# Kernel tuning notes

Hardware: AMD Instinct MI355X
Metric: run time of the kernel (lower is better)

Reference implementation:

```python
import jax, jax.numpy as jnp
import numpy as np

N = 50000   # nodes
E = 600000  # edges (avg degree 12)
D = 128     # embedding_dim == hidden_features
L = 4       # depth


def setup_inputs() -> dict:
    key = jax.random.key(0)
    k0, k1, k2, k3 = jax.random.split(key, 4)
    scale = 1.0 / np.sqrt(D)
    node_embedding = jax.random.normal(k0, (N, D), jnp.float32)
    edge_index = jax.random.randint(k1, (2, E), 0, N, dtype=jnp.int32)
    Ws_rel = jax.random.normal(k2, (L, D, D), jnp.float32) * scale
    bs_rel = jnp.zeros((L, D), jnp.float32)
    Ws_root = jax.random.normal(k3, (L, D, D), jnp.float32) * scale
    return {
        'node_embedding': node_embedding,
        'edge_index': edge_index,
        'Ws_rel': Ws_rel,
        'bs_rel': bs_rel,
        'Ws_root': Ws_root,
    }


def reference(node_embedding, edge_index, Ws_rel, bs_rel, Ws_root):
    # PyG GraphConv (aggr='mean'), flow source_to_target:
    #   out_i = lin_rel(mean_{j in N(i)} x_j) + lin_root(x_i)
    # followed by ELU (dropout probs are 0 -> identity).
    n = node_embedding.shape[0]
    src, dst = edge_index[0], edge_index[1]
    ones = jnp.ones((edge_index.shape[1],), node_embedding.dtype)
    deg = jax.ops.segment_sum(ones, dst, num_segments=n)
    inv_deg = (1.0 / jnp.maximum(deg, 1.0))[:, None]  # [n, 1]
    X = node_embedding
    for l in range(Ws_rel.shape[0]):
        agg = jax.ops.segment_sum(X[src], dst, num_segments=n) * inv_deg  # [n, D]
        out = agg @ Ws_rel[l] + bs_rel[l] + X @ Ws_root[l]
        X = jax.nn.elu(out)
    return X
```

## Files before the change

### kernel.cpp

```cpp
#include <hip/hip_runtime.h>

#define D 128
#define LDR 264
#define SLOTS 64
#define EPB 2048

typedef short bf16x8 __attribute__((ext_vector_type(8)));
typedef float f32x4 __attribute__((ext_vector_type(4)));

__device__ __forceinline__ unsigned short f2bf(float f) {
  unsigned int u = __float_as_uint(f);
  unsigned int r = (u + 0x7fff + ((u >> 16) & 1)) >> 16;
  return (unsigned short)r;
}
__device__ __forceinline__ unsigned int pack2bf(float lo, float hi) {
  return (unsigned int)f2bf(lo) | ((unsigned int)f2bf(hi) << 16);
}

__global__ __launch_bounds__(256) void k_build(
    const int* __restrict__ src, const int* __restrict__ dst, int E, int N,
    int* __restrict__ cursor, unsigned short* __restrict__ csr64,
    const float* __restrict__ X0, unsigned short* __restrict__ Xb, int total4,
    const float* __restrict__ Wrel, const float* __restrict__ Wroot,
    unsigned short* __restrict__ Wp, int wtot,
    int fb, int cb) {
  int b = blockIdx.x;
  if (b < fb) {
    int p = b & 7;
    int chunk = b >> 3;
    int lo = (int)((long long)p * N / 8);
    int hi = (int)((long long)(p + 1) * N / 8);
    int base = chunk * EPB + threadIdx.x;
#pragma unroll
    for (int it = 0; it < EPB / 256; ++it, base += 256) {
      if (base < E) {
        int d = dst[base];
        if (d >= lo && d < hi) {
          int ps = atomicAdd(&cursor[d], 1);
          if (ps < SLOTS) csr64[d * SLOTS + ps] = (unsigned short)src[base];
        }
      }
    }
    return;
  }
  b -= fb;
  if (b < cb) {
    int i = b * 256 + threadIdx.x;
    if (i < total4) {
      float4 v = ((const float4*)X0)[i];
      ushort4 o;
      o.x = f2bf(v.x); o.y = f2bf(v.y); o.z = f2bf(v.z); o.w = f2bf(v.w);
      ((ushort4*)Xb)[i] = o;
    }
    return;
  }
  b -= cb;
  {
    int gid = b * 256 + threadIdx.x;
    if (gid >= wtot) return;
    int lane = gid & 63;
    int t = gid >> 6;
    int ctg = t & 7; t >>= 3;
    int ks = t & 7; t >>= 3;
    int l = t;
    const float* Wr = Wrel + (size_t)l * D * D;
    const float* Wo = Wroot + (size_t)l * D * D;
    int colc = ctg * 16 + (lane & 15);
    int krow0 = ks * 32 + (lane >> 4) * 8;
    unsigned short tmp[8];
#pragma unroll
    for (int j = 0; j < 8; ++j) {
      int kr = krow0 + j;
      float w = (kr < D) ? Wr[(size_t)kr * D + colc] : Wo[(size_t)(kr - D) * D + colc];
      tmp[j] = f2bf(w);
    }
    unsigned short* dstp = Wp + ((size_t)gid) * 8;
#pragma unroll
    for (int j = 0; j < 8; ++j) dstp[j] = tmp[j];
  }
}


#define ACC8(v) \
    acc[0] += __uint_as_float((v).x << 16); acc[1] += __uint_as_float((v).x & 0xffff0000u); \
    acc[2] += __uint_as_float((v).y << 16); acc[3] += __uint_as_float((v).y & 0xffff0000u); \
    acc[4] += __uint_as_float((v).z << 16); acc[5] += __uint_as_float((v).z & 0xffff0000u); \
    acc[6] += __uint_as_float((v).w << 16); acc[7] += __uint_as_float((v).w & 0xffff0000u);

__global__ __launch_bounds__(256) void k_aggregate(const unsigned short* __restrict__ X,
    const int* __restrict__ cursor, const unsigned short* __restrict__ csr64,
    unsigned short* __restrict__ agg, int N) {
  int wave = (int)((blockIdx.x * blockDim.x + threadIdx.x) >> 6);
  int lane = threadIdx.x & 63;
  if (wave >= N) return;
  int grp = lane >> 4;
  int l16 = lane & 15;
  int deg = cursor[wave];
  int n = min(deg, SLOTS);
  int eid = (int)csr64[wave * SLOTS + lane];

  float acc[8];
#pragma unroll
  for (int k = 0; k < 8; ++k) acc[k] = 0.f;

  int j4 = 0;
  for (; j4 + 12 <= n; j4 += 12) {
    int s0 = __shfl(eid, j4 + grp);
    int s1 = __shfl(eid, j4 + 4 + grp);
    int s2 = __shfl(eid, j4 + 8 + grp);
    uint4 v0 = *(const uint4*)(X + (size_t)s0 * D + l16 * 8);
    uint4 v1 = *(const uint4*)(X + (size_t)s1 * D + l16 * 8);
    uint4 v2 = *(const uint4*)(X + (size_t)s2 * D + l16 * 8);
    ACC8(v0) ACC8(v1) ACC8(v2)
  }
  if (j4 + 8 <= n) {
    int s0 = __shfl(eid, j4 + grp);
    int s1 = __shfl(eid, j4 + 4 + grp);
    uint4 v0 = *(const uint4*)(X + (size_t)s0 * D + l16 * 8);
    uint4 v1 = *(const uint4*)(X + (size_t)s1 * D + l16 * 8);
    ACC8(v0) ACC8(v1)
    j4 += 8;
  }
  for (; j4 < n; j4 += 4) {
    int jj = j4 + grp;
    int s = __shfl(eid, jj);
    if (jj < n) {
      uint4 v = *(const uint4*)(X + (size_t)s * D + l16 * 8);
      ACC8(v)
    }
  }

#pragma unroll
  for (int k = 0; k < 8; ++k) {
    acc[k] += __shfl_xor(acc[k], 16);
    acc[k] += __shfl_xor(acc[k], 32);
  }

  if (grp == 0) {
    float inv = 1.0f / fmaxf((float)deg, 1.0f);
    uint4 o;
    o.x = pack2bf(acc[0] * inv, acc[1] * inv);
    o.y = pack2bf(acc[2] * inv, acc[3] * inv);
    o.z = pack2bf(acc[4] * inv, acc[5] * inv);
    o.w = pack2bf(acc[6] * inv, acc[7] * inv);
    *(uint4*)(agg + (size_t)wave * D + l16 * 8) = o;
  }
}

__global__ __launch_bounds__(256, 4) void k_layer(const unsigned short* __restrict__ agg,
    const unsigned short* __restrict__ Xin, const unsigned short* __restrict__ Wp_l,
    const float* __restrict__ bias, unsigned short* __restrict__ Xnext,
    float* __restrict__ out_f32, int last, int N) {
  __shared__ __align__(16) unsigned short sRow[64 * LDR];
  int tid = threadIdx.x;
  int r0 = blockIdx.x * 64;

  for (int i = tid; i < 64 * 32; i += 256) {
    int r = i >> 5, ch = i & 31;
    int row = r0 + r;
    uint4 v = make_uint4(0, 0, 0, 0);
    if (row < N) {
      const unsigned short* srcp = (ch < 16)
          ? (agg + (size_t)row * D + ch * 8)
          : (Xin + (size_t)row * D + (ch - 16) * 8);
      v = *(const uint4*)srcp;
    }
    *(uint4*)(&sRow[r * LDR + ch * 8]) = v;
  }
  __syncthreads();

  int wave = tid >> 6, lane = tid & 63;
  int m = lane & 15, q = lane >> 4;
  int ct0 = wave * 2;

  f32x4 acc[4][2];
#pragma unroll
  for (int g = 0; g < 4; ++g)
#pragma unroll
    for (int c = 0; c < 2; ++c) acc[g][c] = (f32x4){0.f, 0.f, 0.f, 0.f};

  const unsigned short* arow = &sRow[m * LDR + q * 8];
#pragma unroll
  for (int ks = 0; ks < 8; ++ks) {
    bf16x8 b0 = *(const bf16x8*)(Wp_l + ((size_t)((ks * 8 + ct0 + 0) * 64 + lane)) * 8);
    bf16x8 b1 = *(const bf16x8*)(Wp_l + ((size_t)((ks * 8 + ct0 + 1) * 64 + lane)) * 8);
    bf16x8 a0 = *(const bf16x8*)(arow + ks * 32);
    bf16x8 a1 = *(const bf16x8*)(arow + 16 * LDR + ks * 32);
    bf16x8 a2 = *(const bf16x8*)(arow + 32 * LDR + ks * 32);
    bf16x8 a3 = *(const bf16x8*)(arow + 48 * LDR + ks * 32);
    acc[0][0] = __builtin_amdgcn_mfma_f32_16x16x32_bf16(a0, b0, acc[0][0], 0, 0, 0);
    acc[0][1] = __builtin_amdgcn_mfma_f32_16x16x32_bf16(a0, b1, acc[0][1], 0, 0, 0);
    acc[1][0] = __builtin_amdgcn_mfma_f32_16x16x32_bf16(a1, b0, acc[1][0], 0, 0, 0);
    acc[1][1] = __builtin_amdgcn_mfma_f32_16x16x32_bf16(a1, b1, acc[1][1], 0, 0, 0);
    acc[2][0] = __builtin_amdgcn_mfma_f32_16x16x32_bf16(a2, b0, acc[2][0], 0, 0, 0);
    acc[2][1] = __builtin_amdgcn_mfma_f32_16x16x32_bf16(a2, b1, acc[2][1], 0, 0, 0);
    acc[3][0] = __builtin_amdgcn_mfma_f32_16x16x32_bf16(a3, b0, acc[3][0], 0, 0, 0);
    acc[3][1] = __builtin_amdgcn_mfma_f32_16x16x32_bf16(a3, b1, acc[3][1], 0, 0, 0);
  }

#pragma unroll
  for (int g = 0; g < 4; ++g) {
#pragma unroll
    for (int c = 0; c < 2; ++c) {
      int col = (ct0 + c) * 16 + m;
      float bv = bias[col];
      int rbase = r0 + g * 16 + q * 4;
#pragma unroll
      for (int j = 0; j < 4; ++j) {
        int row = rbase + j;
        float v = acc[g][c][j] + bv;
        float e = __expf(fminf(v, 0.f)) - 1.f;
        v = v > 0.f ? v : e;
        if (last) {
          if (row < N) out_f32[(size_t)row * D + col] = v;
        } else {
          unsigned int h = (unsigned int)f2bf(v);
          unsigned int nb = (unsigned int)__shfl_xor((int)h, 1);
          if (!(m & 1) && row < N)
            *(unsigned int*)(Xnext + (size_t)row * D + col) = h | (nb << 16);
        }
      }
    }
  }
}


extern "C" void kernel_launch(void* const* d_in, const int* in_sizes, int n_in,
                              void* d_out, int out_size, void* d_ws, size_t ws_size,
                              hipStream_t stream) {
  const float* X0    = (const float*)d_in[0];
  const int*   eidx  = (const int*)d_in[1];
  const float* Wrel  = (const float*)d_in[2];
  const float* brel  = (const float*)d_in[3];
  const float* Wroot = (const float*)d_in[4];
  float* out = (float*)d_out;

  const int N = in_sizes[0] / D;
  const int E = in_sizes[1] / 2;
  const int L = in_sizes[3] / D;
  const int* src = eidx;
  const int* dst = eidx + E;

  char* ws = (char*)d_ws;
  size_t off = 0;
  auto carve = [&](size_t bytes) -> void* {
    void* p = ws + off;
    off = (off + bytes + 255) & ~(size_t)255;
    return p;
  };
  unsigned short* Xb0  = (unsigned short*)carve((size_t)N * D * sizeof(unsigned short));
  unsigned short* Xb1  = (unsigned short*)carve((size_t)N * D * sizeof(unsigned short));
  unsigned short* aggb = (unsigned short*)carve((size_t)N * D * sizeof(unsigned short));
  unsigned short* Wp   = (unsigned short*)carve((size_t)L * 4096 * 8 * sizeof(unsigned short));
  int*            cursor = (int*)carve((size_t)N * sizeof(int));
  unsigned short* csr64  = (unsigned short*)carve((size_t)N * SLOTS * sizeof(unsigned short));
  (void)ws_size; (void)n_in; (void)out_size;

  hipMemsetAsync(cursor, 0, (size_t)N * sizeof(int), stream);

  const int chunks = (E + EPB - 1) / EPB;
  const int fb = chunks * 8;
  const int total4 = N * D / 4;
  const int cb = (total4 + 255) / 256;
  const int wtot = L * 4096;
  const int wb = (wtot + 255) / 256;
  k_build<<<fb + cb + wb, 256, 0, stream>>>(src, dst, E, N, cursor, csr64,
      X0, Xb0, total4, Wrel, Wroot, Wp, wtot, fb, cb);

  const int ab = (N + 3) / 4;
  const int lb = (N + 63) / 64;

  const unsigned short* Xcur = Xb0;
  for (int l = 0; l < L; ++l) {
    int last = (l == L - 1) ? 1 : 0;
    unsigned short* Xnext = (Xcur == Xb0) ? Xb1 : Xb0;
    k_aggregate<<<ab, 256, 0, stream>>>(Xcur, cursor, csr64, aggb, N);
    k_layer<<<lb, 256, 0, stream>>>(aggb, Xcur, Wp + (size_t)l * 4096 * 8,
        brel + (size_t)l * D, Xnext, out, last, N);
    Xcur = Xnext;
  }
}
```

Measured before the change: 259.4 us.

## Assign one node per 16-lane group in aggregation instead of one per wave

```diff
diff --git a/kernel.cpp b/kernel.cpp
--- a/kernel.cpp
+++ b/kernel.cpp
@@ -90,60 +90,48 @@
 __global__ __launch_bounds__(256) void k_aggregate(const unsigned short* __restrict__ X,
     const int* __restrict__ cursor, const unsigned short* __restrict__ csr64,
     unsigned short* __restrict__ agg, int N) {
-  int wave = (int)((blockIdx.x * blockDim.x + threadIdx.x) >> 6);
+  int wid = (int)((blockIdx.x * blockDim.x + threadIdx.x) >> 6);
   int lane = threadIdx.x & 63;
-  if (wave >= N) return;
-  int grp = lane >> 4;
-  int l16 = lane & 15;
-  int deg = cursor[wave];
+  int g = lane >> 4, l16 = lane & 15;
+  int node = wid * 4 + g;
+  bool valid = node < N;
+  int nv = valid ? node : (N - 1);
+  int deg = cursor[nv];
   int n = min(deg, SLOTS);
-  int eid = (int)csr64[wave * SLOTS + lane];
+  int nmax = n;
+  nmax = max(nmax, __shfl_xor(nmax, 16));
+  nmax = max(nmax, __shfl_xor(nmax, 32));
 
   float acc[8];
 #pragma unroll
   for (int k = 0; k < 8; ++k) acc[k] = 0.f;
 
-  int j4 = 0;
-  for (; j4 + 12 <= n; j4 += 12) {
-    int s0 = __shfl(eid, j4 + grp);
-    int s1 = __shfl(eid, j4 + 4 + grp);
-    int s2 = __shfl(eid, j4 + 8 + grp);
-    uint4 v0 = *(const uint4*)(X + (size_t)s0 * D + l16 * 8);
-    uint4 v1 = *(const uint4*)(X + (size_t)s1 * D + l16 * 8);
-    uint4 v2 = *(const uint4*)(X + (size_t)s2 * D + l16 * 8);
-    ACC8(v0) ACC8(v1) ACC8(v2)
-  }
-  if (j4 + 8 <= n) {
-    int s0 = __shfl(eid, j4 + grp);
-    int s1 = __shfl(eid, j4 + 4 + grp);
-    uint4 v0 = *(const uint4*)(X + (size_t)s0 * D + l16 * 8);
-    uint4 v1 = *(const uint4*)(X + (size_t)s1 * D + l16 * 8);
-    ACC8(v0) ACC8(v1)
-    j4 += 8;
-  }
-  for (; j4 < n; j4 += 4) {
-    int jj = j4 + grp;
-    int s = __shfl(eid, jj);
-    if (jj < n) {
-      uint4 v = *(const uint4*)(X + (size_t)s * D + l16 * 8);
-      ACC8(v)
-    }
-  }
-
-#pragma unroll
-  for (int k = 0; k < 8; ++k) {
-    acc[k] += __shfl_xor(acc[k], 16);
-    acc[k] += __shfl_xor(acc[k], 32);
-  }
-
-  if (grp == 0) {
+  const unsigned short* bucket = csr64 + (size_t)nv * SLOTS;
+  for (int j0 = 0; j0 < nmax; j0 += 16) {
+    int ew = (int)bucket[j0 + l16];
+#pragma unroll
+    for (int jj = 0; jj < 16; jj += 2) {
+      int s0 = __shfl(ew, g * 16 + jj);
+      int s1 = __shfl(ew, g * 16 + jj + 1);
+      if (j0 + jj < n) {
+        uint4 v0 = *(const uint4*)(X + (size_t)s0 * D + l16 * 8);
+        ACC8(v0)
+      }
+      if (j0 + jj + 1 < n) {
+        uint4 v1 = *(const uint4*)(X + (size_t)s1 * D + l16 * 8);
+        ACC8(v1)
+      }
+    }
+  }
+
+  if (valid) {
     float inv = 1.0f / fmaxf((float)deg, 1.0f);
     uint4 o;
     o.x = pack2bf(acc[0] * inv, acc[1] * inv);
     o.y = pack2bf(acc[2] * inv, acc[3] * inv);
     o.z = pack2bf(acc[4] * inv, acc[5] * inv);
     o.w = pack2bf(acc[6] * inv, acc[7] * inv);
-    *(uint4*)(agg + (size_t)wave * D + l16 * 8) = o;
+    *(uint4*)(agg + (size_t)node * D + l16 * 8) = o;
   }
 }
 
@@ -267,7 +255,7 @@
   k_build<<<fb + cb + wb, 256, 0, stream>>>(src, dst, E, N, cursor, csr64,
       X0, Xb0, total4, Wrel, Wroot, Wp, wtot, fb, cb);
 
-  const int ab = (N + 3) / 4;
+  const int ab = (N + 15) / 16;
   const int lb = (N + 63) / 64;
 
   const unsigned short* Xcur = Xb0;
```

After: 275.7 us. 1.06x slower.

## Fuse all build, aggregate and layer kernels into one cooperative persistent kernel

Applied to the files above, without the earlier changes.

```diff
diff --git a/kernel.cpp b/kernel.cpp
--- a/kernel.cpp
+++ b/kernel.cpp
@@ -1,4 +1,7 @@
 #include <hip/hip_runtime.h>
+#include <hip/hip_cooperative_groups.h>
+
+namespace cg = cooperative_groups;
 
 #define D 128
 #define LDR 264
@@ -17,14 +20,13 @@
   return (unsigned int)f2bf(lo) | ((unsigned int)f2bf(hi) << 16);
 }
 
-__global__ __launch_bounds__(256) void k_build(
+
+__device__ __forceinline__ void build_body(int b,
     const int* __restrict__ src, const int* __restrict__ dst, int E, int N,
     int* __restrict__ cursor, unsigned short* __restrict__ csr64,
     const float* __restrict__ X0, unsigned short* __restrict__ Xb, int total4,
     const float* __restrict__ Wrel, const float* __restrict__ Wroot,
-    unsigned short* __restrict__ Wp, int wtot,
-    int fb, int cb) {
-  int b = blockIdx.x;
+    unsigned short* __restrict__ Wp, int wtot, int fb, int cb) {
   if (b < fb) {
     int p = b & 7;
     int chunk = b >> 3;
@@ -80,17 +82,16 @@
   }
 }
 
-
 #define ACC8(v) \
     acc[0] += __uint_as_float((v).x << 16); acc[1] += __uint_as_float((v).x & 0xffff0000u); \
     acc[2] += __uint_as_float((v).y << 16); acc[3] += __uint_as_float((v).y & 0xffff0000u); \
     acc[4] += __uint_as_float((v).z << 16); acc[5] += __uint_as_float((v).z & 0xffff0000u); \
     acc[6] += __uint_as_float((v).w << 16); acc[7] += __uint_as_float((v).w & 0xffff0000u);
 
-__global__ __launch_bounds__(256) void k_aggregate(const unsigned short* __restrict__ X,
-    const int* __restrict__ cursor, const unsigned short* __restrict__ csr64,
-    unsigned short* __restrict__ agg, int N) {
-  int wave = (int)((blockIdx.x * blockDim.x + threadIdx.x) >> 6);
+__device__ __forceinline__ void aggregate_body(int vb,
+    const unsigned short* __restrict__ X, const int* __restrict__ cursor,
+    const unsigned short* __restrict__ csr64, unsigned short* __restrict__ agg, int N) {
+  int wave = vb * 4 + (int)(threadIdx.x >> 6);
   int lane = threadIdx.x & 63;
   if (wave >= N) return;
   int grp = lane >> 4;
@@ -147,13 +148,13 @@
   }
 }
 
-__global__ __launch_bounds__(256, 4) void k_layer(const unsigned short* __restrict__ agg,
-    const unsigned short* __restrict__ Xin, const unsigned short* __restrict__ Wp_l,
-    const float* __restrict__ bias, unsigned short* __restrict__ Xnext,
-    float* __restrict__ out_f32, int last, int N) {
-  __shared__ __align__(16) unsigned short sRow[64 * LDR];
+__device__ __forceinline__ void layer_body(int vb,
+    const unsigned short* __restrict__ agg, const unsigned short* __restrict__ Xin,
+    const unsigned short* __restrict__ Wp_l, const float* __restrict__ bias,
+    unsigned short* __restrict__ Xnext, float* __restrict__ out_f32,
+    int last, int N, unsigned short* sRow) {
   int tid = threadIdx.x;
-  int r0 = blockIdx.x * 64;
+  int r0 = vb * 64;
 
   for (int i = tid; i < 64 * 32; i += 256) {
     int r = i >> 5, ch = i & 31;
@@ -225,6 +226,77 @@
 }
 
 
+struct KParams {
+  const int* src; const int* dst; int E; int N;
+  int* cursor; unsigned short* csr64;
+  const float* X0; unsigned short* Xb0; unsigned short* Xb1; unsigned short* aggb;
+  int total4;
+  const float* Wrel; const float* Wroot; const float* brel;
+  unsigned short* Wp; int wtot;
+  int fb, cb;
+  float* out; int L;
+  int bt;
+  int ab, lb;
+};
+
+__global__ __launch_bounds__(256, 4) void k_all(KParams p) {
+  cg::grid_group grid = cg::this_grid();
+  __shared__ __align__(16) unsigned short sRow[64 * LDR];
+  int nb = gridDim.x;
+
+  for (int i = blockIdx.x * 256 + threadIdx.x; i < p.N; i += nb * 256) p.cursor[i] = 0;
+  grid.sync();
+
+  for (int vb = blockIdx.x; vb < p.bt; vb += nb)
+    build_body(vb, p.src, p.dst, p.E, p.N, p.cursor, p.csr64,
+               p.X0, p.Xb0, p.total4, p.Wrel, p.Wroot, p.Wp, p.wtot, p.fb, p.cb);
+  grid.sync();
+
+  const unsigned short* Xcur = p.Xb0;
+  for (int l = 0; l < p.L; ++l) {
+    for (int vb = blockIdx.x; vb < p.ab; vb += nb)
+      aggregate_body(vb, Xcur, p.cursor, p.csr64, p.aggb, p.N);
+    grid.sync();
+
+    int last = (l == p.L - 1) ? 1 : 0;
+    unsigned short* Xnext = (Xcur == p.Xb0) ? p.Xb1 : p.Xb0;
+    const unsigned short* WpL = p.Wp + (size_t)l * 4096 * 8;
+    const float* bias = p.brel + (size_t)l * D;
+    for (int vb = blockIdx.x; vb < p.lb; vb += nb) {
+      layer_body(vb, p.aggb, Xcur, WpL, bias, Xnext, p.out, last, p.N, sRow);
+      __syncthreads();
+    }
+    if (!last) grid.sync();
+    Xcur = Xnext;
+  }
+}
+
+
+__global__ __launch_bounds__(256) void k_build(
+    const int* __restrict__ src, const int* __restrict__ dst, int E, int N,
+    int* __restrict__ cursor, unsigned short* __restrict__ csr64,
+    const float* __restrict__ X0, unsigned short* __restrict__ Xb, int total4,
+    const float* __restrict__ Wrel, const float* __restrict__ Wroot,
+    unsigned short* __restrict__ Wp, int wtot, int fb, int cb) {
+  build_body(blockIdx.x, src, dst, E, N, cursor, csr64, X0, Xb, total4,
+             Wrel, Wroot, Wp, wtot, fb, cb);
+}
+
+__global__ __launch_bounds__(256) void k_aggregate(const unsigned short* __restrict__ X,
+    const int* __restrict__ cursor, const unsigned short* __restrict__ csr64,
+    unsigned short* __restrict__ agg, int N) {
+  aggregate_body(blockIdx.x, X, cursor, csr64, agg, N);
+}
+
+__global__ __launch_bounds__(256, 4) void k_layer(const unsigned short* __restrict__ agg,
+    const unsigned short* __restrict__ Xin, const unsigned short* __restrict__ Wp_l,
+    const float* __restrict__ bias, unsigned short* __restrict__ Xnext,
+    float* __restrict__ out_f32, int last, int N) {
+  __shared__ __align__(16) unsigned short sRow[64 * LDR];
+  layer_body(blockIdx.x, agg, Xin, Wp_l, bias, Xnext, out_f32, last, N, sRow);
+}
+
+
 extern "C" void kernel_launch(void* const* d_in, const int* in_sizes, int n_in,
                               void* d_out, int out_size, void* d_ws, size_t ws_size,
                               hipStream_t stream) {
@@ -256,27 +328,51 @@
   unsigned short* csr64  = (unsigned short*)carve((size_t)N * SLOTS * sizeof(unsigned short));
   (void)ws_size; (void)n_in; (void)out_size;
 
-  hipMemsetAsync(cursor, 0, (size_t)N * sizeof(int), stream);
-
   const int chunks = (E + EPB - 1) / EPB;
   const int fb = chunks * 8;
   const int total4 = N * D / 4;
   const int cb = (total4 + 255) / 256;
   const int wtot = L * 4096;
   const int wb = (wtot + 255) / 256;
-  k_build<<<fb + cb + wb, 256, 0, stream>>>(src, dst, E, N, cursor, csr64,
-      X0, Xb0, total4, Wrel, Wroot, Wp, wtot, fb, cb);
-
+  const int bt = fb + cb + wb;
   const int ab = (N + 3) / 4;
   const int lb = (N + 63) / 64;
 
-  const unsigned short* Xcur = Xb0;
-  for (int l = 0; l < L; ++l) {
-    int last = (l == L - 1) ? 1 : 0;
-    unsigned short* Xnext = (Xcur == Xb0) ? Xb1 : Xb0;
-    k_aggregate<<<ab, 256, 0, stream>>>(Xcur, cursor, csr64, aggb, N);
-    k_layer<<<lb, 256, 0, stream>>>(aggb, Xcur, Wp + (size_t)l * 4096 * 8,
-        brel + (size_t)l * D, Xnext, out, last, N);
-    Xcur = Xnext;
-  }
-}
+  int maxb = 0;
+  hipError_t oerr = hipOccupancyMaxActiveBlocksPerMultiprocessor(
+      &maxb, (const void*)k_all, 256, 0);
+  bool coop_ok = false;
+  if (oerr == hipSuccess && maxb >= 1) {
+    int grid = maxb * 256;
+    if (grid > ab) grid = ab;
+    KParams p;
+    p.src = src; p.dst = dst; p.E = E; p.N = N;
+    p.cursor = cursor; p.csr64 = csr64;
+    p.X0 = X0; p.Xb0 = Xb0; p.Xb1 = Xb1; p.aggb = aggb;
+    p.total4 = total4;
+    p.Wrel = Wrel; p.Wroot = Wroot; p.brel = brel;
+    p.Wp = Wp; p.wtot = wtot;
+    p.fb = fb; p.cb = cb;
+    p.out = out; p.L = L;
+    p.bt = bt; p.ab = ab; p.lb = lb;
+    void* args[] = {&p};
+    hipError_t lerr = hipLaunchCooperativeKernel((const void*)k_all, dim3(grid),
+                                                 dim3(256), args, 0, stream);
+    coop_ok = (lerr == hipSuccess);
+  }
+
+  if (!coop_ok) {
+    hipMemsetAsync(cursor, 0, (size_t)N * sizeof(int), stream);
+    k_build<<<bt, 256, 0, stream>>>(src, dst, E, N, cursor, csr64,
+        X0, Xb0, total4, Wrel, Wroot, Wp, wtot, fb, cb);
+    const unsigned short* Xcur = Xb0;
+    for (int l = 0; l < L; ++l) {
+      int last = (l == L - 1) ? 1 : 0;
+      unsigned short* Xnext = (Xcur == Xb0) ? Xb1 : Xb0;
+      k_aggregate<<<ab, 256, 0, stream>>>(Xcur, cursor, csr64, aggb, N);
+      k_layer<<<lb, 256, 0, stream>>>(aggb, Xcur, Wp + (size_t)l * 4096 * 8,
+          brel + (size_t)l * D, Xnext, out, last, N);
+      Xcur = Xnext;
+    }
+  }
+}
```

New measurement: 870.6 us. 3.36x slower.
